# Kernel tuning notes

Hardware: AMD Instinct MI355X
Metric: run time of the kernel (lower is better)

The kernel has to match this reference:

```python
import jax, jax.numpy as jnp
import numpy as np

B, T, D, H = 2, 2048, 1024, 16
DK = D // H


def setup_inputs() -> dict:
    key = jax.random.key(0)
    ks = jax.random.split(key, 13)
    s = 1.0 / np.sqrt(D)
    return {
        "q": jax.random.normal(ks[0], (B, T, D), jnp.float32),
        "k": jax.random.normal(ks[1], (B, T, D), jnp.float32),
        "v": jax.random.normal(ks[2], (B, T, D), jnp.float32),
        "mask": jax.random.randint(ks[3], (B, T, T), 0, 2, jnp.int32),
        "Wq": jax.random.normal(ks[4], (D, D), jnp.float32) * s,
        "bq": jax.random.normal(ks[5], (D,), jnp.float32) * s,
        "Wk": jax.random.normal(ks[6], (D, D), jnp.float32) * s,
        "bk": jax.random.normal(ks[7], (D,), jnp.float32) * s,
        "Wv": jax.random.normal(ks[8], (D, D), jnp.float32) * s,
        "bv": jax.random.normal(ks[9], (D,), jnp.float32) * s,
        "Wo": jax.random.normal(ks[10], (D, D), jnp.float32) * s,
        "bo": jax.random.normal(ks[11], (D,), jnp.float32) * s,
    }


def reference(q, k, v, mask, Wq, bq, Wk, bk, Wv, bv, Wo, bo):
    # Linear projections (torch Linear: x @ W.T + b), split into heads.
    Q = (q @ Wq.T + bq).reshape(B, T, H, DK).transpose(0, 2, 1, 3)  # [B,H,Tq,dk]
    K = (k @ Wk.T + bk).reshape(B, T, H, DK).transpose(0, 2, 1, 3)
    V = (v @ Wv.T + bv).reshape(B, T, H, DK).transpose(0, 2, 1, 3)
    scores = jnp.einsum("bhqd,bhkd->bhqk", Q, K) / jnp.sqrt(jnp.float32(DK))
    # 3-dim mask path: mask==0 -> -1e9, broadcast over heads.
    scores = jnp.where(mask[:, None, :, :] == 0, jnp.float32(-1e9), scores)
    attn = jax.nn.softmax(scores, axis=-1)
    out = jnp.einsum("bhqk,bhkd->bhqd", attn, V)  # [B,H,Tq,dk]
    out = out.transpose(0, 2, 1, 3).reshape(B, T, D)
    return out @ Wo.T + bo
```

## Files before the change

kernel.cpp:

```cpp
#include <hip/hip_runtime.h>
#include <cstdint>
#include <cstddef>

#define TSEQ 2048
#define DMOD 1024
#define NHEAD 16
#define NBATCH 2
#define MT (NBATCH * TSEQ)
#define LOG2E 1.44269504088896340736f

typedef __attribute__((ext_vector_type(8))) __bf16 bf16x8;
typedef __attribute__((ext_vector_type(4))) float f32x4;
typedef __attribute__((ext_vector_type(8))) unsigned short u16x8;
typedef __attribute__((ext_vector_type(4))) unsigned short u16x4;
typedef __attribute__((ext_vector_type(4))) uint32_t u32x4;

__device__ __forceinline__ unsigned short f2bf(float f) {
  uint32_t u = __builtin_bit_cast(uint32_t, f);
  u += 0x7fffu + ((u >> 16) & 1u);
  return (unsigned short)(u >> 16);
}

__device__ __forceinline__ uint32_t cvt_pk_bf16(float a, float b) {
  uint32_t r;
  asm("v_cvt_pk_bf16_f32 %0, %1, %2" : "=v"(r) : "v"(a), "v"(b));
  return r;
}

__device__ __forceinline__ void gload_lds16(const void* g, const void* l) {
  auto gp = (const __attribute__((address_space(1))) uint32_t*)((uintptr_t)g);
  auto lp = (__attribute__((address_space(3))) uint32_t*)((uintptr_t)l);
  __builtin_amdgcn_global_load_lds(gp, lp, 16, 0, 0);
}

__global__ __launch_bounds__(256) void cvt_wm(const float* __restrict__ w0,
                                              const float* __restrict__ w1,
                                              const float* __restrict__ w2,
                                              const float* __restrict__ w3,
                                              const int* __restrict__ m,
                                              unsigned short* __restrict__ dw,
                                              uint32_t* __restrict__ mx) {
  const int bx = blockIdx.x;
  if (bx < 4096) {
    const size_t idx = ((size_t)bx * 256 + threadIdx.x) * 4;
    const int wsel = (int)(idx >> 20);
    const float* s = wsel == 0 ? w0 : (wsel == 1 ? w1 : (wsel == 2 ? w2 : w3));
    const float4 t = *(const float4*)(s + (idx & 0xFFFFFu));
    u16x4 o;
    o[0] = f2bf(t.x); o[1] = f2bf(t.y); o[2] = f2bf(t.z); o[3] = f2bf(t.w);
    *(u16x4*)(dw + idx) = o;
  } else {
    const size_t W = (size_t)(bx - 4096) * 256 + threadIdx.x;
    const int hi = (int)((W >> 3) & 3), ct = (int)(W & 7);
    const size_t bqkt = W >> 5;
    const int kt = (int)(bqkt & 15);
    const size_t bq = bqkt >> 4;
    const int4 mm = *(const int4*)(m + bq * TSEQ + kt * 128 + ct * 16 + hi * 4);
    const uint32_t o = (mm.x ? 0xFFu : 0u) | (mm.y ? 0xFF00u : 0u) |
                       (mm.z ? 0xFF0000u : 0u) | (mm.w ? 0xFF000000u : 0u);
    mx[W] = o;
  }
}

__device__ __forceinline__ void store_c(unsigned short* C, size_t idx, float v) { C[idx] = f2bf(v); }
__device__ __forceinline__ void store_c(float* C, size_t idx, float v) { C[idx] = v; }

template <typename OT, int MF, bool AF32>
__global__ __launch_bounds__(256) void gemm_bt(const void* __restrict__ A0v,
                                               const void* __restrict__ A1v,
                                               const void* __restrict__ A2v,
                                               const unsigned short* __restrict__ W0,
                                               const unsigned short* __restrict__ W1,
                                               const unsigned short* __restrict__ W2,
                                               const float* __restrict__ b0,
                                               const float* __restrict__ b1,
                                               const float* __restrict__ b2,
                                               OT* __restrict__ C0, OT* __restrict__ C1, OT* __restrict__ C2,
                                               float s0, float s1, float s2) {
  constexpr int BM = MF * 32;
  constexpr int NX = 4096 / BM;
  const int nb = gridDim.x, per = nb >> 3, bid = blockIdx.x;
  const int swz = (bid & 7) * per + (bid >> 3);
  const int z = swz / (NX * 8);
  const int rem = swz % (NX * 8);
  const int m0 = (rem >> 3) * BM, n0 = (rem & 7) * 128;

  const void* Av = z == 0 ? A0v : (z == 1 ? A1v : A2v);
  const unsigned short* Bw = z == 0 ? W0 : (z == 1 ? W1 : W2);
  const float* bias = z == 0 ? b0 : (z == 1 ? b1 : b2);
  OT* C = z == 0 ? C0 : (z == 1 ? C1 : C2);
  const float scale = z == 0 ? s0 : (z == 1 ? s1 : s2);

  __shared__ alignas(16) unsigned short As[2][BM * 32];
  __shared__ alignas(16) unsigned short Bs[2][128 * 32];
  const int tid = threadIdx.x;
  const int wid = tid >> 6;
  const int lane = tid & 63;
  const int lo = lane & 15, hi = lane >> 4;
  const int wr = wid >> 1, wc = wid & 1;
  f32x4 acc[MF][4] = {};

  const int r0 = tid >> 2, c8 = (tid & 3) * 8;
  float4 fa[2][2];

  auto loadA = [&](int k0) {
    if constexpr (AF32) {
#pragma unroll
      for (int i = 0; i < 2; ++i) {
        const int chunk = i * 256 + tid;
        const int row = chunk >> 2, cc = (chunk & 3) * 8;
        const float* p = (const float*)Av + (size_t)(m0 + row) * DMOD + k0 + cc;
        fa[i][0] = *(const float4*)p;
        fa[i][1] = *(const float4*)(p + 4);
      }
    }
  };
  auto writeA = [&](int buf) {
    if constexpr (AF32) {
#pragma unroll
      for (int i = 0; i < 2; ++i) {
        const int chunk = i * 256 + tid;
        u32x4 o;
        o[0] = cvt_pk_bf16(fa[i][0].x, fa[i][0].y);
        o[1] = cvt_pk_bf16(fa[i][0].z, fa[i][0].w);
        o[2] = cvt_pk_bf16(fa[i][1].x, fa[i][1].y);
        o[3] = cvt_pk_bf16(fa[i][1].z, fa[i][1].w);
        *(u32x4*)((char*)As + buf * (BM * 64) + chunk * 16) = o;
      }
    }
  };
  auto stage = [&](int buf, int k0) {
#pragma unroll
    for (int i = 0; i < 2; ++i) {
      const int chunk = i * 256 + tid;
      if constexpr (!AF32) {
        if (i < MF / 2)
          gload_lds16((const unsigned short*)Av + (size_t)(m0 + i * 64 + r0) * DMOD + k0 + c8,
                      (const char*)As + buf * (BM * 64) + chunk * 16);
      }
      gload_lds16(Bw + (size_t)(n0 + i * 64 + r0) * DMOD + k0 + c8,
                  (const char*)Bs + buf * 8192 + chunk * 16);
    }
  };

  loadA(0);
  writeA(0);
  stage(0, 0);
  __syncthreads();

  for (int k0 = 0; k0 < DMOD; k0 += 32) {
    const int cur = (k0 >> 5) & 1;
    const bool more = k0 + 32 < DMOD;
    if (more) { loadA(k0 + 32); stage(cur ^ 1, k0 + 32); }

    bf16x8 af[MF], bfr[4];
#pragma unroll
    for (int m = 0; m < MF; ++m)
      af[m] = *(const bf16x8*)((const char*)As + cur * (BM * 64) +
                               (wr * (MF * 16) + m * 16 + lo) * 64 + hi * 16);
#pragma unroll
    for (int n = 0; n < 4; ++n)
      bfr[n] = *(const bf16x8*)((const char*)Bs + cur * 8192 +
                                (wc * 64 + n * 16 + lo) * 64 + hi * 16);
#pragma unroll
    for (int m = 0; m < MF; ++m)
#pragma unroll
      for (int n = 0; n < 4; ++n)
        acc[m][n] = __builtin_amdgcn_mfma_f32_16x16x32_bf16(af[m], bfr[n], acc[m][n], 0, 0, 0);

    if (more) writeA(cur ^ 1);
    __syncthreads();
  }

#pragma unroll
  for (int n = 0; n < 4; ++n) {
    const int col = n0 + wc * 64 + n * 16 + lo;
    const float bv = bias[col];
#pragma unroll
    for (int m = 0; m < MF; ++m) {
      const int row = m0 + wr * (MF * 16) + m * 16 + hi * 4;
#pragma unroll
      for (int r = 0; r < 4; ++r)
        store_c(C, (size_t)(row + r) * DMOD + col, (acc[m][n][r] + bv) * scale);
    }
  }
}

__global__ __launch_bounds__(256) void transpose_v(const unsigned short* __restrict__ Vp,
                                                   unsigned short* __restrict__ Vt) {
  __shared__ alignas(16) unsigned short tile[64][72];
  const int tid = threadIdx.x;
  const int bt0 = blockIdx.x * 64;
  const int h = blockIdx.y;
  const int b = bt0 >> 11;
  const int t0 = bt0 & (TSEQ - 1);
#pragma unroll
  for (int i = 0; i < 2; ++i) {
    const int chunk = i * 256 + tid;
    const int row = chunk >> 3, c = chunk & 7;
    *(uint4*)((char*)&tile[row][0] + c * 16) =
        *(const uint4*)(Vp + (size_t)(bt0 + row) * DMOD + h * 64 + c * 8);
  }
  __syncthreads();
#pragma unroll
  for (int i = 0; i < 2; ++i) {
    const int chunk = i * 256 + tid;
    const int dk = chunk >> 3, c = chunk & 7;
    u16x8 o;
#pragma unroll
    for (int j = 0; j < 8; ++j) {
      const int x = c * 8 + j;
      const int kl = (x & 32) | ((x & 24) >> 1) | ((x & 4) << 2) | (x & 3);
      o[j] = tile[kl][dk];
    }
    *(u16x8*)(Vt + ((size_t)(b * NHEAD + h) * 64 + dk) * TSEQ + t0 + c * 8) = o;
  }
}

__global__ __launch_bounds__(512, 4) void attn_kernel(const unsigned short* __restrict__ Qp,
                                                      const unsigned short* __restrict__ Kp,
                                                      const unsigned short* __restrict__ Vt,
                                                      const uint32_t* __restrict__ mx,
                                                      unsigned short* __restrict__ AO) {
  __shared__ alignas(16) unsigned short Ks[2][128 * 64];
  __shared__ alignas(16) unsigned short Vs[2][64 * 128];
  const int tid = threadIdx.x;
  const int w = tid >> 6, lane = tid & 63;
  const int lo = lane & 15, hi = lane >> 4;
  const int f = blockIdx.x;
  const int swz = (f & 7) * 64 + (f >> 3);
  const int q0 = (swz & 15) * 128;
  const int h = (swz >> 4) & 15;
  const int b = swz >> 8;

  bf16x8 qf[2];
  {
    const unsigned short* qsrc =
        Qp + (size_t)(b * TSEQ + q0 + w * 16 + lo) * DMOD + h * 64 + hi * 8;
    qf[0] = *(const bf16x8*)qsrc;
    qf[1] = *(const bf16x8*)(qsrc + 32);
  }

  bf16x8 ones;
  {
    u32x4 od;
    od[0] = 0x3F803F80u; od[1] = 0x3F803F80u; od[2] = 0x3F803F80u; od[3] = 0x3F803F80u;
    ones = __builtin_bit_cast(bf16x8, od);
  }

  f32x4 o_acc[4] = {};
  f32x4 l_acc = {};

  const size_t kbase = (size_t)(b * TSEQ) * DMOD + h * 64;
  const size_t vbase = (size_t)(b * NHEAD + h) * 64 * TSEQ;

  const int c0 = tid, c1 = 512 + tid;
  const unsigned short* kp0 = Kp + kbase + (size_t)(c0 >> 3) * DMOD + ((c0 & 7) ^ ((c0 >> 3) & 7)) * 8;
  const unsigned short* kp1 = Kp + kbase + (size_t)(c1 >> 3) * DMOD + ((c1 & 7) ^ ((c1 >> 3) & 7)) * 8;
  const unsigned short* vp0 = Vt + vbase + (size_t)(c0 >> 4) * TSEQ + ((c0 & 15) ^ ((c0 >> 4) & 7)) * 8;
  const unsigned short* vp1 = Vt + vbase + (size_t)(c1 >> 4) * TSEQ + ((c1 & 15) ^ ((c1 >> 4) & 7)) * 8;
  const uint32_t* mp = mx + (size_t)(b * TSEQ + q0 + w * 16 + lo) * 512 + hi * 8;
  const int wb0 = c0 * 16, wb1 = c1 * 16;

  int koffA[8], koffB[8];
#pragma unroll
  for (int ct = 0; ct < 8; ++ct) {
    const int kcol = ct * 16 + lo;
    koffA[ct] = kcol * 128 + ((hi ^ (kcol & 7)) * 16);
    koffB[ct] = kcol * 128 + (((4 + hi) ^ (kcol & 7)) * 16);
  }
  int voff[4][4];
#pragma unroll
  for (int vt = 0; vt < 4; ++vt) {
    const int dk = vt * 16 + lo;
#pragma unroll
    for (int c = 0; c < 4; ++c) voff[vt][c] = dk * 256 + (((c * 4 + hi) ^ (dk & 7)) * 16);
  }

  auto stage = [&](int buf) {
    gload_lds16(kp0, (const char*)Ks[buf] + wb0);
    gload_lds16(kp1, (const char*)Ks[buf] + wb1);
    gload_lds16(vp0, (const char*)Vs[buf] + wb0);
    gload_lds16(vp1, (const char*)Vs[buf] + wb1);
    kp0 += (size_t)128 * DMOD; kp1 += (size_t)128 * DMOD;
    vp0 += 128; vp1 += 128;
  };

  const uint32_t selA = 0x01010000u, selB = 0x03030202u;
  const int NT = TSEQ / 128;

  uint4 mc0 = *(const uint4*)mp, mc1 = *(const uint4*)(mp + 4);
  mp += 32;
  stage(0);
  __syncthreads();

  for (int kt = 0; kt < NT; ++kt) {
    uint4 mn0 = mc0, mn1 = mc1;
    if (kt + 1 < NT) {
      mn0 = *(const uint4*)mp;
      mn1 = *(const uint4*)(mp + 4);
      mp += 32;
      stage((kt + 1) & 1);
    }

    const char* ksb = (const char*)Ks[kt & 1];
    const char* vsb = (const char*)Vs[kt & 1];
    f32x4 s[8];
    __builtin_amdgcn_s_setprio(1);
#pragma unroll
    for (int ct = 0; ct < 8; ++ct) {
      bf16x8 kf0 = *(const bf16x8*)(ksb + koffA[ct]);
      bf16x8 kf1 = *(const bf16x8*)(ksb + koffB[ct]);
      f32x4 zz = {0.f, 0.f, 0.f, 0.f};
      s[ct] = __builtin_amdgcn_mfma_f32_16x16x32_bf16(kf0, qf[0], zz, 0, 0, 0);
      s[ct] = __builtin_amdgcn_mfma_f32_16x16x32_bf16(kf1, qf[1], s[ct], 0, 0, 0);
    }
    __builtin_amdgcn_s_setprio(0);

#pragma unroll
    for (int ct = 0; ct < 8; ++ct) {
      s[ct][0] = __builtin_exp2f(s[ct][0]);
      s[ct][1] = __builtin_exp2f(s[ct][1]);
      s[ct][2] = __builtin_exp2f(s[ct][2]);
      s[ct][3] = __builtin_exp2f(s[ct][3]);
    }

    bf16x8 pf[4];
#pragma unroll
    for (int c = 0; c < 4; ++c) {
      const uint32_t We = c == 0 ? mc0.x : (c == 1 ? mc0.z : (c == 2 ? mc1.x : mc1.z));
      const uint32_t Wo = c == 0 ? mc0.y : (c == 1 ? mc0.w : (c == 2 ? mc1.y : mc1.w));
      u32x4 pd;
      pd[0] = cvt_pk_bf16(s[2 * c][0], s[2 * c][1]) & __builtin_amdgcn_perm(We, We, selA);
      pd[1] = cvt_pk_bf16(s[2 * c][2], s[2 * c][3]) & __builtin_amdgcn_perm(We, We, selB);
      pd[2] = cvt_pk_bf16(s[2 * c + 1][0], s[2 * c + 1][1]) & __builtin_amdgcn_perm(Wo, Wo, selA);
      pd[3] = cvt_pk_bf16(s[2 * c + 1][2], s[2 * c + 1][3]) & __builtin_amdgcn_perm(Wo, Wo, selB);
      pf[c] = __builtin_bit_cast(bf16x8, pd);
    }

    __builtin_amdgcn_s_setprio(1);
#pragma unroll
    for (int vt = 0; vt < 4; ++vt) {
#pragma unroll
      for (int c = 0; c < 4; ++c) {
        bf16x8 vf = *(const bf16x8*)(vsb + voff[vt][c]);
        o_acc[vt] = __builtin_amdgcn_mfma_f32_16x16x32_bf16(pf[c], vf, o_acc[vt], 0, 0, 0);
      }
    }
#pragma unroll
    for (int c = 0; c < 4; ++c)
      l_acc = __builtin_amdgcn_mfma_f32_16x16x32_bf16(pf[c], ones, l_acc, 0, 0, 0);
    __builtin_amdgcn_s_setprio(0);

    __syncthreads();
    mc0 = mn0; mc1 = mn1;
  }

#pragma unroll
  for (int r = 0; r < 4; ++r) {
    const float rl = 1.0f / l_acc[r];
    const size_t orow = (size_t)(b * TSEQ + q0 + w * 16 + hi * 4 + r) * DMOD + h * 64;
#pragma unroll
    for (int vt = 0; vt < 4; ++vt)
      AO[orow + vt * 16 + lo] = f2bf(o_acc[vt][r] * rl);
  }
}

extern "C" void kernel_launch(void* const* d_in, const int* in_sizes, int n_in,
                              void* d_out, int out_size, void* d_ws, size_t ws_size,
                              hipStream_t stream) {
  const float* q  = (const float*)d_in[0];
  const float* k  = (const float*)d_in[1];
  const float* v  = (const float*)d_in[2];
  const int* mask = (const int*)d_in[3];
  const float* Wq = (const float*)d_in[4];
  const float* bq = (const float*)d_in[5];
  const float* Wk = (const float*)d_in[6];
  const float* bk = (const float*)d_in[7];
  const float* Wv = (const float*)d_in[8];
  const float* bv = (const float*)d_in[9];
  const float* Wo = (const float*)d_in[10];
  const float* bo = (const float*)d_in[11];
  float* out = (float*)d_out;

  char* ws = (char*)d_ws;
  const size_t SZ_BT = (size_t)MT * DMOD * 2;

  unsigned short* Qp  = (unsigned short*)(ws + 0);
  unsigned short* Kp  = (unsigned short*)(ws + SZ_BT);
  unsigned short* Vp  = (unsigned short*)(ws + 2 * SZ_BT);
  unsigned short* Vt  = (unsigned short*)(ws + 3 * SZ_BT);
  unsigned short* Wqb = (unsigned short*)(ws + 4 * SZ_BT);
  uint32_t*       mx  = (uint32_t*)(ws + 5 * SZ_BT);
  unsigned short* AO  = Vp;
  unsigned short* Wob = Wqb + 3 * DMOD * DMOD;

  const int nW = DMOD * DMOD;

  cvt_wm<<<dim3(4096 + (NBATCH * TSEQ * 16 * 32) / 256), 256, 0, stream>>>(
      Wq, Wk, Wv, Wo, mask, Wqb, mx);

  const float qs = 0.125f * LOG2E;
  gemm_bt<unsigned short, 4, true><<<dim3(768), 256, 0, stream>>>(
      q, k, v, Wqb, Wqb + nW, Wqb + 2 * nW, bq, bk, bv, Qp, Kp, Vp, qs, 1.0f, 1.0f);

  transpose_v<<<dim3(MT / 64, NHEAD), 256, 0, stream>>>(Vp, Vt);

  attn_kernel<<<dim3(512), 512, 0, stream>>>(Qp, Kp, Vt, mx, AO);

  gemm_bt<float, 2, false><<<dim3(512), 256, 0, stream>>>(
      AO, AO, AO, Wob, Wob, Wob, bo, bo, bo, out, out, out, 1.0f, 1.0f, 1.0f);
}
```

Measured before the change: 140.3 us.

## Software-pipeline attention: overlap next tile's QK with current exp/PV

Restructures the attention key loop so the QK^T MFMAs for tile kt+1 are issued alongside the exp/mask/PV work for tile kt. Two score register sets alternate, and V gets a triple-buffered LDS stage so V data stays live one tile longer. Also replaces the koffB table with an XOR of koffA and tidies the GEMM A/B staging indices. This is meant to hide the exp/convert latency behind matrix work, at the cost of more registers and LDS, which may cut occupancy.

```diff
diff --git a/kernel.cpp b/kernel.cpp
--- a/kernel.cpp
+++ b/kernel.cpp
@@ -79,6 +79,7 @@
                                                float s0, float s1, float s2) {
   constexpr int BM = MF * 32;
   constexpr int NX = 4096 / BM;
+  constexpr int ACH = MF / 2;
   const int nb = gridDim.x, per = nb >> 3, bid = blockIdx.x;
   const int swz = (bid & 7) * per + (bid >> 3);
   const int z = swz / (NX * 8);
@@ -100,31 +101,30 @@
   const int wr = wid >> 1, wc = wid & 1;
   f32x4 acc[MF][4] = {};
 
-  const int r0 = tid >> 2, c8 = (tid & 3) * 8;
-  float4 fa[2][2];
+  float4 fa[ACH][2];
 
   auto loadA = [&](int k0) {
     if constexpr (AF32) {
 #pragma unroll
-      for (int i = 0; i < 2; ++i) {
-        const int chunk = i * 256 + tid;
+      for (int j = 0; j < ACH; ++j) {
+        const int chunk = j * 256 + tid;
         const int row = chunk >> 2, cc = (chunk & 3) * 8;
         const float* p = (const float*)Av + (size_t)(m0 + row) * DMOD + k0 + cc;
-        fa[i][0] = *(const float4*)p;
-        fa[i][1] = *(const float4*)(p + 4);
+        fa[j][0] = *(const float4*)p;
+        fa[j][1] = *(const float4*)(p + 4);
       }
     }
   };
   auto writeA = [&](int buf) {
     if constexpr (AF32) {
 #pragma unroll
-      for (int i = 0; i < 2; ++i) {
-        const int chunk = i * 256 + tid;
+      for (int j = 0; j < ACH; ++j) {
+        const int chunk = j * 256 + tid;
         u32x4 o;
-        o[0] = cvt_pk_bf16(fa[i][0].x, fa[i][0].y);
-        o[1] = cvt_pk_bf16(fa[i][0].z, fa[i][0].w);
-        o[2] = cvt_pk_bf16(fa[i][1].x, fa[i][1].y);
-        o[3] = cvt_pk_bf16(fa[i][1].z, fa[i][1].w);
+        o[0] = cvt_pk_bf16(fa[j][0].x, fa[j][0].y);
+        o[1] = cvt_pk_bf16(fa[j][0].z, fa[j][0].w);
+        o[2] = cvt_pk_bf16(fa[j][1].x, fa[j][1].y);
+        o[3] = cvt_pk_bf16(fa[j][1].z, fa[j][1].w);
         *(u32x4*)((char*)As + buf * (BM * 64) + chunk * 16) = o;
       }
     }
@@ -133,12 +133,13 @@
 #pragma unroll
     for (int i = 0; i < 2; ++i) {
       const int chunk = i * 256 + tid;
+      const int row = chunk >> 2, c8 = (chunk & 3) * 8;
       if constexpr (!AF32) {
-        if (i < MF / 2)
-          gload_lds16((const unsigned short*)Av + (size_t)(m0 + i * 64 + r0) * DMOD + k0 + c8,
+        if (i < ACH)
+          gload_lds16((const unsigned short*)Av + (size_t)(m0 + row) * DMOD + k0 + c8,
                       (const char*)As + buf * (BM * 64) + chunk * 16);
       }
-      gload_lds16(Bw + (size_t)(n0 + i * 64 + r0) * DMOD + k0 + c8,
+      gload_lds16(Bw + (size_t)(n0 + row) * DMOD + k0 + c8,
                   (const char*)Bs + buf * 8192 + chunk * 16);
     }
   };
@@ -223,7 +224,7 @@
                                                       const uint32_t* __restrict__ mx,
                                                       unsigned short* __restrict__ AO) {
   __shared__ alignas(16) unsigned short Ks[2][128 * 64];
-  __shared__ alignas(16) unsigned short Vs[2][64 * 128];
+  __shared__ alignas(16) unsigned short Vs[3][64 * 128];
   const int tid = threadIdx.x;
   const int w = tid >> 6, lane = tid & 63;
   const int lo = lane & 15, hi = lane >> 4;
@@ -262,12 +263,11 @@
   const uint32_t* mp = mx + (size_t)(b * TSEQ + q0 + w * 16 + lo) * 512 + hi * 8;
   const int wb0 = c0 * 16, wb1 = c1 * 16;
 
-  int koffA[8], koffB[8];
+  int koffA[8];
 #pragma unroll
   for (int ct = 0; ct < 8; ++ct) {
     const int kcol = ct * 16 + lo;
     koffA[ct] = kcol * 128 + ((hi ^ (kcol & 7)) * 16);
-    koffB[ct] = kcol * 128 + (((4 + hi) ^ (kcol & 7)) * 16);
   }
   int voff[4][4];
 #pragma unroll
@@ -277,46 +277,31 @@
     for (int c = 0; c < 4; ++c) voff[vt][c] = dk * 256 + (((c * 4 + hi) ^ (dk & 7)) * 16);
   }
 
-  auto stage = [&](int buf) {
-    gload_lds16(kp0, (const char*)Ks[buf] + wb0);
-    gload_lds16(kp1, (const char*)Ks[buf] + wb1);
-    gload_lds16(vp0, (const char*)Vs[buf] + wb0);
-    gload_lds16(vp1, (const char*)Vs[buf] + wb1);
+  auto stage = [&](int kbuf, int vbuf) {
+    gload_lds16(kp0, (const char*)Ks[kbuf] + wb0);
+    gload_lds16(kp1, (const char*)Ks[kbuf] + wb1);
+    gload_lds16(vp0, (const char*)Vs[vbuf] + wb0);
+    gload_lds16(vp1, (const char*)Vs[vbuf] + wb1);
     kp0 += (size_t)128 * DMOD; kp1 += (size_t)128 * DMOD;
     vp0 += 128; vp1 += 128;
   };
 
   const uint32_t selA = 0x01010000u, selB = 0x03030202u;
-  const int NT = TSEQ / 128;
-
-  uint4 mc0 = *(const uint4*)mp, mc1 = *(const uint4*)(mp + 4);
-  mp += 32;
-  stage(0);
-  __syncthreads();
-
-  for (int kt = 0; kt < NT; ++kt) {
-    uint4 mn0 = mc0, mn1 = mc1;
-    if (kt + 1 < NT) {
-      mn0 = *(const uint4*)mp;
-      mn1 = *(const uint4*)(mp + 4);
-      mp += 32;
-      stage((kt + 1) & 1);
-    }
-
-    const char* ksb = (const char*)Ks[kt & 1];
-    const char* vsb = (const char*)Vs[kt & 1];
-    f32x4 s[8];
+
+  auto QK = [&](f32x4* s, const char* ksb) {
     __builtin_amdgcn_s_setprio(1);
 #pragma unroll
     for (int ct = 0; ct < 8; ++ct) {
       bf16x8 kf0 = *(const bf16x8*)(ksb + koffA[ct]);
-      bf16x8 kf1 = *(const bf16x8*)(ksb + koffB[ct]);
+      bf16x8 kf1 = *(const bf16x8*)(ksb + (koffA[ct] ^ 64));
       f32x4 zz = {0.f, 0.f, 0.f, 0.f};
       s[ct] = __builtin_amdgcn_mfma_f32_16x16x32_bf16(kf0, qf[0], zz, 0, 0, 0);
       s[ct] = __builtin_amdgcn_mfma_f32_16x16x32_bf16(kf1, qf[1], s[ct], 0, 0, 0);
     }
     __builtin_amdgcn_s_setprio(0);
-
+  };
+
+  auto EXPPV = [&](f32x4* s, uint4 mc0, uint4 mc1, const char* vsb) {
 #pragma unroll
     for (int ct = 0; ct < 8; ++ct) {
       s[ct][0] = __builtin_exp2f(s[ct][0]);
@@ -324,7 +309,6 @@
       s[ct][2] = __builtin_exp2f(s[ct][2]);
       s[ct][3] = __builtin_exp2f(s[ct][3]);
     }
-
     bf16x8 pf[4];
 #pragma unroll
     for (int c = 0; c < 4; ++c) {
@@ -337,7 +321,6 @@
       pd[3] = cvt_pk_bf16(s[2 * c + 1][2], s[2 * c + 1][3]) & __builtin_amdgcn_perm(Wo, Wo, selB);
       pf[c] = __builtin_bit_cast(bf16x8, pd);
     }
-
     __builtin_amdgcn_s_setprio(1);
 #pragma unroll
     for (int vt = 0; vt < 4; ++vt) {
@@ -351,10 +334,35 @@
     for (int c = 0; c < 4; ++c)
       l_acc = __builtin_amdgcn_mfma_f32_16x16x32_bf16(pf[c], ones, l_acc, 0, 0, 0);
     __builtin_amdgcn_s_setprio(0);
-
+  };
+
+  const int NT = TSEQ / 128;
+  f32x4 sA[8], sB[8];
+  uint4 mA0, mA1, mB0, mB1;
+
+  mA0 = *(const uint4*)mp; mA1 = *(const uint4*)(mp + 4); mp += 32;
+  stage(0, 0);
+  __syncthreads();
+  stage(1, 1);
+  QK(sA, (const char*)Ks[0]);
+  __syncthreads();
+
+  for (int kt = 1; kt < NT; kt += 2) {
+    mB0 = *(const uint4*)mp; mB1 = *(const uint4*)(mp + 4); mp += 32;
+    if (kt + 1 < NT) stage((kt + 1) & 1, (kt + 1) % 3);
+    QK(sB, (const char*)Ks[1]);
+    EXPPV(sA, mA0, mA1, (const char*)Vs[(kt - 1) % 3]);
     __syncthreads();
-    mc0 = mn0; mc1 = mn1;
-  }
+
+    if (kt + 1 < NT) {
+      mA0 = *(const uint4*)mp; mA1 = *(const uint4*)(mp + 4); mp += 32;
+      if (kt + 2 < NT) stage((kt + 2) & 1, (kt + 2) % 3);
+      QK(sA, (const char*)Ks[0]);
+      EXPPV(sB, mB0, mB1, (const char*)Vs[kt % 3]);
+      __syncthreads();
+    }
+  }
+  EXPPV(sB, mB0, mB1, (const char*)Vs[(NT - 1) % 3]);
 
 #pragma unroll
   for (int r = 0; r < 4; ++r) {
```

Result: slower. 223.5 us (+59.3%).

## Double GEMM K-tile to 64 and XOR-swizzle LDS layout

Applied to the files above, without the earlier changes.

The projection GEMM now stages a K depth of 64 per iteration instead of 32, which halves the number of barriers and loop iterations. Each row in LDS becomes 128 bytes, and 16-byte chunks are XOR-swizzled by row so that MFMA fragment reads avoid bank conflicts. The cost is twice the LDS footprint, which may reduce occupancy, plus more registers to hold the prefetched fp32 A data.

```diff
diff --git a/kernel.cpp b/kernel.cpp
--- a/kernel.cpp
+++ b/kernel.cpp
@@ -91,8 +91,8 @@
   OT* C = z == 0 ? C0 : (z == 1 ? C1 : C2);
   const float scale = z == 0 ? s0 : (z == 1 ? s1 : s2);
 
-  __shared__ alignas(16) unsigned short As[2][BM * 32];
-  __shared__ alignas(16) unsigned short Bs[2][128 * 32];
+  __shared__ alignas(16) unsigned short As[2][BM * 64];
+  __shared__ alignas(16) unsigned short Bs[2][128 * 64];
   const int tid = threadIdx.x;
   const int wid = tid >> 6;
   const int lane = tid & 63;
@@ -100,46 +100,50 @@
   const int wr = wid >> 1, wc = wid & 1;
   f32x4 acc[MF][4] = {};
 
-  const int r0 = tid >> 2, c8 = (tid & 3) * 8;
-  float4 fa[2][2];
+  float4 fa[MF][2];
 
   auto loadA = [&](int k0) {
     if constexpr (AF32) {
 #pragma unroll
-      for (int i = 0; i < 2; ++i) {
-        const int chunk = i * 256 + tid;
-        const int row = chunk >> 2, cc = (chunk & 3) * 8;
-        const float* p = (const float*)Av + (size_t)(m0 + row) * DMOD + k0 + cc;
-        fa[i][0] = *(const float4*)p;
-        fa[i][1] = *(const float4*)(p + 4);
+      for (int j = 0; j < MF; ++j) {
+        const int chunk = j * 256 + tid;
+        const int row = chunk >> 3, cl = (chunk & 7) ^ (row & 7);
+        const float* p = (const float*)Av + (size_t)(m0 + row) * DMOD + k0 + cl * 8;
+        fa[j][0] = *(const float4*)p;
+        fa[j][1] = *(const float4*)(p + 4);
       }
     }
   };
   auto writeA = [&](int buf) {
     if constexpr (AF32) {
 #pragma unroll
-      for (int i = 0; i < 2; ++i) {
-        const int chunk = i * 256 + tid;
+      for (int j = 0; j < MF; ++j) {
+        const int chunk = j * 256 + tid;
         u32x4 o;
-        o[0] = cvt_pk_bf16(fa[i][0].x, fa[i][0].y);
-        o[1] = cvt_pk_bf16(fa[i][0].z, fa[i][0].w);
-        o[2] = cvt_pk_bf16(fa[i][1].x, fa[i][1].y);
-        o[3] = cvt_pk_bf16(fa[i][1].z, fa[i][1].w);
-        *(u32x4*)((char*)As + buf * (BM * 64) + chunk * 16) = o;
+        o[0] = cvt_pk_bf16(fa[j][0].x, fa[j][0].y);
+        o[1] = cvt_pk_bf16(fa[j][0].z, fa[j][0].w);
+        o[2] = cvt_pk_bf16(fa[j][1].x, fa[j][1].y);
+        o[3] = cvt_pk_bf16(fa[j][1].z, fa[j][1].w);
+        *(u32x4*)((char*)As + buf * (BM * 128) + chunk * 16) = o;
       }
     }
   };
   auto stage = [&](int buf, int k0) {
-#pragma unroll
-    for (int i = 0; i < 2; ++i) {
+    if constexpr (!AF32) {
+#pragma unroll
+      for (int i = 0; i < MF; ++i) {
+        const int chunk = i * 256 + tid;
+        const int row = chunk >> 3, cl = (chunk & 7) ^ (row & 7);
+        gload_lds16((const unsigned short*)Av + (size_t)(m0 + row) * DMOD + k0 + cl * 8,
+                    (const char*)As + buf * (BM * 128) + chunk * 16);
+      }
+    }
+#pragma unroll
+    for (int i = 0; i < 4; ++i) {
       const int chunk = i * 256 + tid;
-      if constexpr (!AF32) {
-        if (i < MF / 2)
-          gload_lds16((const unsigned short*)Av + (size_t)(m0 + i * 64 + r0) * DMOD + k0 + c8,
-                      (const char*)As + buf * (BM * 64) + chunk * 16);
-      }
-      gload_lds16(Bw + (size_t)(n0 + i * 64 + r0) * DMOD + k0 + c8,
-                  (const char*)Bs + buf * 8192 + chunk * 16);
+      const int row = chunk >> 3, cl = (chunk & 7) ^ (row & 7);
+      gload_lds16(Bw + (size_t)(n0 + row) * DMOD + k0 + cl * 8,
+                  (const char*)Bs + buf * 16384 + chunk * 16);
     }
   };
 
@@ -148,25 +152,32 @@
   stage(0, 0);
   __syncthreads();
 
-  for (int k0 = 0; k0 < DMOD; k0 += 32) {
-    const int cur = (k0 >> 5) & 1;
-    const bool more = k0 + 32 < DMOD;
-    if (more) { loadA(k0 + 32); stage(cur ^ 1, k0 + 32); }
-
-    bf16x8 af[MF], bfr[4];
-#pragma unroll
-    for (int m = 0; m < MF; ++m)
-      af[m] = *(const bf16x8*)((const char*)As + cur * (BM * 64) +
-                               (wr * (MF * 16) + m * 16 + lo) * 64 + hi * 16);
-#pragma unroll
-    for (int n = 0; n < 4; ++n)
-      bfr[n] = *(const bf16x8*)((const char*)Bs + cur * 8192 +
-                                (wc * 64 + n * 16 + lo) * 64 + hi * 16);
-#pragma unroll
-    for (int m = 0; m < MF; ++m)
-#pragma unroll
-      for (int n = 0; n < 4; ++n)
-        acc[m][n] = __builtin_amdgcn_mfma_f32_16x16x32_bf16(af[m], bfr[n], acc[m][n], 0, 0, 0);
+  for (int k0 = 0; k0 < DMOD; k0 += 64) {
+    const int cur = (k0 >> 6) & 1;
+    const bool more = k0 + 64 < DMOD;
+    if (more) { loadA(k0 + 64); stage(cur ^ 1, k0 + 64); }
+
+#pragma unroll
+    for (int kk = 0; kk < 2; ++kk) {
+      bf16x8 af[MF], bfr[4];
+#pragma unroll
+      for (int m = 0; m < MF; ++m) {
+        const int row = wr * (MF * 16) + m * 16 + lo;
+        af[m] = *(const bf16x8*)((const char*)As + cur * (BM * 128) +
+                                 row * 128 + (((kk * 4 + hi) ^ (lo & 7)) * 16));
+      }
+#pragma unroll
+      for (int n = 0; n < 4; ++n) {
+        const int row = wc * 64 + n * 16 + lo;
+        bfr[n] = *(const bf16x8*)((const char*)Bs + cur * 16384 +
+                                  row * 128 + (((kk * 4 + hi) ^ (lo & 7)) * 16));
+      }
+#pragma unroll
+      for (int m = 0; m < MF; ++m)
+#pragma unroll
+        for (int n = 0; n < 4; ++n)
+          acc[m][n] = __builtin_amdgcn_mfma_f32_16x16x32_bf16(af[m], bfr[n], acc[m][n], 0, 0, 0);
+    }
 
     if (more) writeA(cur ^ 1);
     __syncthreads();
```

After: 138.8 us (median of 2 runs). About the same (-1.0%).
